# Kernel optimization log

Measured on AMD Instinct MI355X. Metric: run time of the kernel, lower is better.

## Reference

```python
import jax, jax.numpy as jnp
import numpy as np

THETA = 10000.0
NUM_HEADS = 16
MAX_SEQ_LEN = 2048

def _rope_tables(d_k, max_seq_len, theta=THETA):
    dims = jnp.arange(0, d_k, 2, dtype=jnp.float32)
    freqs = 1.0 / theta ** (dims / d_k)
    t = jnp.arange(max_seq_len, dtype=jnp.float32)
    angles = jnp.outer(t, freqs)  # (max_seq_len, d_k//2)
    return jnp.cos(angles), jnp.sin(angles)

def _apply_rope(x, token_positions, cos_tab, sin_tab):
    # x: (..., seq_len, d_k)
    cos = jnp.repeat(cos_tab[token_positions], 2, axis=-1)  # (seq_len, d_k)
    sin = jnp.repeat(sin_tab[token_positions], 2, axis=-1)
    # interleaved rotate-half: (-x1, x0, -x3, x2, ...)
    xp = x.reshape(*x.shape[:-1], -1, 2)
    x_neg = jnp.stack([-xp[..., 1], xp[..., 0]], axis=-1).reshape(x.shape)
    return x * cos + x_neg * sin

def setup_inputs() -> dict:
    key = jax.random.key(0)
    ks = jax.random.split(key, 5)
    B, S, D = 4, 2048, 1024
    scale = 1.0 / np.sqrt(D)
    return {
        "x": jax.random.normal(ks[0], (B, S, D), dtype=jnp.float32),
        "q_proj": jax.random.normal(ks[1], (D, D), dtype=jnp.float32) * scale,
        "k_proj": jax.random.normal(ks[2], (D, D), dtype=jnp.float32) * scale,
        "v_proj": jax.random.normal(ks[3], (D, D), dtype=jnp.float32) * scale,
        "o_proj": jax.random.normal(ks[4], (D, D), dtype=jnp.float32) * scale,
        "token_positions": jnp.arange(S, dtype=jnp.int64),
    }

def reference(x, q_proj, k_proj, v_proj, o_proj, token_positions):
    B, S, D = x.shape
    H = NUM_HEADS
    d_k = D // H
    cos_tab, sin_tab = _rope_tables(d_k, MAX_SEQ_LEN)

    q = (x @ q_proj).reshape(B, S, H, d_k).transpose(0, 2, 1, 3)  # (B,H,S,d_k)
    k = (x @ k_proj).reshape(B, S, H, d_k).transpose(0, 2, 1, 3)
    v = (x @ v_proj).reshape(B, S, H, d_k).transpose(0, 2, 1, 3)

    q = _apply_rope(q, token_positions, cos_tab, sin_tab)
    k = _apply_rope(k, token_positions, cos_tab, sin_tab)

    scores = jnp.einsum('bhqd,bhkd->bhqk', q, k) / jnp.sqrt(jnp.float32(d_k))
    causal = jnp.tril(jnp.ones((S, S), dtype=bool))
    scores = jnp.where(causal, scores, -jnp.inf)
    attn = jax.nn.softmax(scores, axis=-1)
    out = jnp.einsum('bhqk,bhkd->bhqd', attn, v)  # (B,H,S,d_k)
    out = out.transpose(0, 2, 1, 3).reshape(B, S, D)
    return out @ o_proj
```

## Files before the change

### kernel.cpp

```cpp
#include <hip/hip_runtime.h>
#include <hip/hip_bf16.h>
#include <stdint.h>


typedef __attribute__((ext_vector_type(8))) short short8;
typedef __attribute__((ext_vector_type(4))) float floatx4;
typedef __attribute__((ext_vector_type(16))) float floatx16;

#define MFMA16(a,b,c) __builtin_amdgcn_mfma_f32_16x16x32_bf16((a),(b),(c),0,0,0)
#define MFMA32(a,b,c) __builtin_amdgcn_mfma_f32_32x32x16_bf16((a),(b),(c),0,0,0)
#define BAR() __builtin_amdgcn_s_barrier()
#define LGKM0 asm volatile("s_waitcnt lgkmcnt(0)" ::: "memory")
#define VMCNT6 asm volatile("s_waitcnt vmcnt(6)" ::: "memory")

__device__ __forceinline__ uint32_t fbits(float f){ uint32_t u; __builtin_memcpy(&u,&f,4); return u; }
__device__ __forceinline__ unsigned short f2bf(float f) {
    uint32_t u = fbits(f);
    return (unsigned short)((u + 0x7fffu + ((u>>16)&1u)) >> 16);
}
__device__ __forceinline__ float bf2f(unsigned short s){ uint32_t u = (uint32_t)s<<16; float f; __builtin_memcpy(&f,&u,4); return f; }
__device__ __forceinline__ uint32_t pkbf(float lo, float hi) {
#if __has_builtin(__builtin_amdgcn_cvt_pk_bf16_f32)
    auto r = __builtin_amdgcn_cvt_pk_bf16_f32(lo, hi);
    uint32_t u; __builtin_memcpy(&u, &r, sizeof(u));
    return u;
#else
    return __builtin_amdgcn_perm(fbits(hi)+0x8000u, fbits(lo)+0x8000u, 0x07060302u);
#endif
}
__device__ __forceinline__ float fexp2(float x) {
#if __has_builtin(__builtin_amdgcn_exp2f)
    return __builtin_amdgcn_exp2f(x);
#else
    return exp2f(x);
#endif
}

__device__ __forceinline__ void load_lds16(const unsigned short* g, unsigned short* l) {
    __builtin_amdgcn_global_load_lds(
        (const __attribute__((address_space(1))) void*)g,
        (__attribute__((address_space(3))) void*)l, 16, 0, 0);
}

__device__ __forceinline__ bool sniff_f32(const unsigned short* xr) {
    int lane = threadIdx.x & 63;
    int bad = 0;
#pragma unroll
    for (int i = 0; i < 16; i++) {
        float v = bf2f(xr[lane * 16 + i]);
        if (!(__builtin_fabsf(v) < 1e10f)) bad = 1;
    }
    return __ballot(bad != 0) != 0ull;
}

__global__ __launch_bounds__(256) void prep_k(
    const void* __restrict__ x,
    const void* __restrict__ wq, const void* __restrict__ wk,
    const void* __restrict__ wv, const void* __restrict__ wo,
    unsigned short* __restrict__ WT, unsigned short* __restrict__ WoT,
    float2* __restrict__ tab, unsigned short* __restrict__ xb) {
    int blk = blockIdx.x, t = threadIdx.x;
    bool f32 = sniff_f32((const unsigned short*)x);
    if (blk < 4096) {
        __shared__ unsigned short tile[32][33];
        int mat = blk >> 10, r = blk & 1023;
        const void* src = (mat == 0) ? wq : (mat == 1) ? wk : (mat == 2) ? wv : wo;
        unsigned short* dst = (mat < 3) ? (WT + (size_t)mat * 1048576) : WoT;
        int bx = (r & 31) * 32, by = (r >> 5) * 32;
        int tx = t & 31, ty = t >> 5;
#pragma unroll
        for (int j = 0; j < 32; j += 8) {
            size_t idx = (size_t)(by + ty + j) * 1024 + bx + tx;
            float v = f32 ? ((const float*)src)[idx] : bf2f(((const unsigned short*)src)[idx]);
            tile[ty + j][tx] = f2bf(v);
        }
        __syncthreads();
#pragma unroll
        for (int j = 0; j < 32; j += 8)
            dst[(size_t)(bx + ty + j) * 1024 + by + tx] = tile[tx][ty + j];
    } else if (blk < 4352) {
        int i = (blk - 4096) * 256 + t;
        int pos = i >> 5, j = i & 31;
        float freq = exp2f(-(float)(2 * j) * (1.0f / 64.0f) * 13.287712379549449f);
        float a = (float)pos * freq;
        tab[i] = make_float2(cosf(a), sinf(a));
    } else {
        size_t base = (size_t)(blk - 4352) * 2048 + (size_t)t * 8;
        if (f32) {
            const float4* s4 = (const float4*)((const float*)x + base);
            float4 a = s4[0], b = s4[1];
            uint4 o;
            o.x = pkbf(a.x, a.y); o.y = pkbf(a.z, a.w);
            o.z = pkbf(b.x, b.y); o.w = pkbf(b.z, b.w);
            *(uint4*)(xb + base) = o;
        } else {
            *(uint4*)(xb + base) = *(const uint4*)((const unsigned short*)x + base);
        }
    }
}

template <int MODE>
__global__ __launch_bounds__(256, 2) void gemmt(
    const unsigned short* __restrict__ A,
    const unsigned short* __restrict__ Bt,
    void* __restrict__ C0,
    unsigned short* __restrict__ C1,
    unsigned short* __restrict__ C2,
    const float2* __restrict__ tab,
    const unsigned short* __restrict__ xsniff) {
    const int K = 1024;
    extern __shared__ __align__(16) char smraw[];
    unsigned short* SL = (unsigned short*)smraw;

    int t = threadIdx.x;
    int lane = t & 63, w = t >> 6;
    int quad = lane >> 4, l15 = lane & 15;
    int wn = w * 64;

    int nbx = gridDim.x;
    int flat = blockIdx.y * nbx + blockIdx.x;
    int cpx = (nbx * gridDim.y) >> 3;
    int swzid = (flat & 7) * cpx + (flat >> 3);
    int bx = swzid % nbx, by = swzid / nbx;
    int m0 = by * 128, n0 = bx * 256;

    floatx4 acc[8][4];
#pragma unroll
    for (int i = 0; i < 8; i++)
#pragma unroll
        for (int j = 0; j < 4; j++) acc[i][j] = (floatx4){0.f, 0.f, 0.f, 0.f};

    int sg = ((t & 3) ^ ((t >> 3) & 3)) * 8;
    const unsigned short* gA = A + (size_t)(m0 + (t >> 2)) * K + sg;
    const unsigned short* gB = Bt + (size_t)(n0 + (t >> 2)) * K + sg;

    int colsw = (quad ^ ((l15 >> 1) & 3)) * 8;

#pragma unroll
    for (int kt = 0; kt < 2; kt++) {
        unsigned short* Sb = SL + kt * 12288 + w * 512;
        load_lds16(gA + kt * 32, Sb);
        load_lds16(gA + (size_t)64 * K + kt * 32, Sb + 2048);
        load_lds16(gB + kt * 32, Sb + 4096);
        load_lds16(gB + (size_t)64 * K + kt * 32, Sb + 6144);
        load_lds16(gB + (size_t)128 * K + kt * 32, Sb + 8192);
        load_lds16(gB + (size_t)192 * K + kt * 32, Sb + 10240);
    }
    VMCNT6;
    __syncthreads();

    int cur = 0, nxt = 2;
#pragma unroll 1
    for (int kt = 0; kt < 32; kt++) {
        const unsigned short* cA = SL + cur * 12288;
        const unsigned short* cB = SL + cur * 12288 + 4096;
        unsigned short* Sb = SL + nxt * 12288 + w * 512;
        int kc = (kt < 30) ? (kt + 2) : 31;
        size_t ko = (size_t)kc * 32;
        short8 af[4], bf[4];

#pragma unroll
        for (int m = 0; m < 4; m++)
            af[m] = *(const short8*)(cA + (m * 16 + l15) * 32 + colsw);
#pragma unroll
        for (int n = 0; n < 4; n++)
            bf[n] = *(const short8*)(cB + (wn + n * 16 + l15) * 32 + colsw);
        load_lds16(gA + ko, Sb);
        load_lds16(gA + (size_t)64 * K + ko, Sb + 2048);
        load_lds16(gB + ko, Sb + 4096);
        BAR(); LGKM0;
        __builtin_amdgcn_s_setprio(1);
#pragma unroll
        for (int m = 0; m < 4; m++)
#pragma unroll
            for (int n = 0; n < 4; n++) acc[m][n] = MFMA16(af[m], bf[n], acc[m][n]);
        __builtin_amdgcn_s_setprio(0);
        BAR();

#pragma unroll
        for (int m = 0; m < 4; m++)
            af[m] = *(const short8*)(cA + ((m + 4) * 16 + l15) * 32 + colsw);
        load_lds16(gB + (size_t)64 * K + ko, Sb + 6144);
        load_lds16(gB + (size_t)128 * K + ko, Sb + 8192);
        load_lds16(gB + (size_t)192 * K + ko, Sb + 10240);
        BAR(); LGKM0;
        __builtin_amdgcn_s_setprio(1);
#pragma unroll
        for (int m = 0; m < 4; m++)
#pragma unroll
            for (int n = 0; n < 4; n++) acc[m + 4][n] = MFMA16(af[m], bf[n], acc[m + 4][n]);
        __builtin_amdgcn_s_setprio(0);
        VMCNT6;
        BAR();

        cur = (cur == 2) ? 0 : cur + 1;
        nxt = (nxt == 2) ? 0 : nxt + 1;
    }

    bool out_f32 = (MODE == 0) ? sniff_f32(xsniff) : false;
#pragma unroll
    for (int i = 0; i < 8; i++) {
#pragma unroll
        for (int j = 0; j < 4; j++) {
            int col = n0 + wn + j * 16 + l15;
            int row0 = m0 + i * 16 + quad * 4;
            if (MODE == 0) {
#pragma unroll
                for (int r = 0; r < 4; r++) {
                    size_t idx = (size_t)(row0 + r) * 1024 + col;
                    if (out_f32) ((float*)C0)[idx] = acc[i][j][r];
                    else ((unsigned short*)C0)[idx] = f2bf(acc[i][j][r]);
                }
            } else {
                int which = col >> 10, nn = col & 1023;
                int b = row0 >> 11, s0 = row0 & 2047;
                if (which == 2) {
                    int hh = nn >> 6, d = nn & 63;
                    uint32_t lo = pkbf(acc[i][j][0], acc[i][j][1]);
                    uint32_t hi = pkbf(acc[i][j][2], acc[i][j][3]);
                    *(uint64_t*)(C2 + ((size_t)((b * 16 + hh) * 64 + d)) * 2048 + s0) =
                        (uint64_t)lo | ((uint64_t)hi << 32);
                } else {
                    int d = nn & 63;
                    unsigned short* dst = (which == 0) ? (unsigned short*)C0 : C1;
                    float sc = (which == 0) ? 0.18033688011112042f : 1.0f;
#pragma unroll
                    for (int r = 0; r < 4; r++) {
                        int s = s0 + r;
                        float v = acc[i][j][r];
                        float pv = __shfl_xor(v, 1);
                        float2 cs = tab[(s << 5) + (d >> 1)];
                        float o = (d & 1) ? (v * cs.x + pv * cs.y) : (v * cs.x - pv * cs.y);
                        dst[((size_t)(b * 2048 + s)) * 1024 + nn] = f2bf(o * sc);
                    }
                }
            }
        }
    }
}

__global__ __launch_bounds__(512, 4) void flash_k(
    const unsigned short* __restrict__ Qb,
    const unsigned short* __restrict__ Kb,
    const unsigned short* __restrict__ Vt,
    unsigned short* __restrict__ A2) {
    __shared__ __align__(16) char sm[33792];
    unsigned short* Kl = (unsigned short*)sm;
    unsigned short* Vl = (unsigned short*)(sm + 16384);
    float4* Osw = (float4*)sm;
    float*  lsw = (float*)(sm + 32768);

    int bh = blockIdx.x;
    int y = blockIdx.y;
    int qt = (y < 8) ? (15 - y) : (y - 8);
    int b = bh >> 4, h = bh & 15;
    int t = threadIdx.x, lane = t & 63, w = t >> 6;
    int wq = w & 3, wg = w >> 2;
    int l31 = lane & 31, half = lane >> 5;
    size_t base = ((size_t)b * 2048) * 1024 + h * 64;
    int q0w = qt * 128 + wq * 32;

    short8 Qf[4];
#pragma unroll
    for (int ks = 0; ks < 4; ks++)
        Qf[ks] = *(const short8*)(Qb + base + (size_t)(q0w + l31) * 1024 + ks * 16 + half * 8);

    floatx16 O[2];
    O[0] = (floatx16)0.0f; O[1] = (floatx16)0.0f;
    float lsum = 0.f;

    int nk = 2 * (qt + 1);

    int srow = t >> 3, gs = t & 7;
    const unsigned short* kg = Kb + base + (size_t)srow * 1024 + gs * 8;
    const unsigned short* vg = Vt + ((size_t)(bh * 64 + srow)) * 2048 + gs * 8;
    int sw = srow * 64 + ((gs ^ (srow & 7)) * 8);

    short8 rk = *(const short8*)(kg);
    short8 rv = *(const short8*)(vg);

    for (int kt = 0; kt < nk; kt++) {
        int k0 = kt * 64, bf = kt & 1;
        *(short8*)&Kl[bf * 4096 + sw] = rk;
        *(short8*)&Vl[bf * 4096 + sw] = rv;
        __syncthreads();
        if (kt + 1 < nk) {
            size_t ko = (size_t)(kt + 1) * 64;
            rk = *(const short8*)(kg + ko * 1024);
            rv = *(const short8*)(vg + ko);
        }
        int k0mb = k0 + wg * 32;
        if (k0mb < q0w + 32) {
            const unsigned short* Klb = Kl + bf * 4096;
            const unsigned short* Vlb = Vl + bf * 4096;
            short8 Ka[4];
#pragma unroll
            for (int ks = 0; ks < 4; ks++)
                Ka[ks] = *(const short8*)&Klb[(wg * 32 + l31) * 64 +
                                              (((ks * 2 + half) ^ (l31 & 7)) * 8)];
            floatx16 Sc = (floatx16)0.0f;
#pragma unroll
            for (int ks = 0; ks < 4; ks++)
                Sc = MFMA32(Ka[ks], Qf[ks], Sc);

            bool domask = (k0mb + 31 > q0w);
            int thr = q0w + l31 - k0mb - half * 4;
            float p[16];
#pragma unroll
            for (int e = 0; e < 16; e++) {
                float v = fexp2(Sc[e]);
                if (domask) {
                    const int ce = (e & 3) + ((e >> 2) << 3);
                    v = (ce > thr) ? 0.f : v;
                }
                p[e] = v;
            }
            float t0 = (p[0] + p[1]) + (p[2] + p[3]);
            float t1 = (p[4] + p[5]) + (p[6] + p[7]);
            float t2 = (p[8] + p[9]) + (p[10] + p[11]);
            float t3 = (p[12] + p[13]) + (p[14] + p[15]);
            lsum += (t0 + t1) + (t2 + t3);
            uint32_t pkm[8];
#pragma unroll
            for (int jj = 0; jj < 8; jj++)
                pkm[jj] = pkbf(p[2 * jj], p[2 * jj + 1]);

            short8 Va[2][2];
#pragma unroll
            for (int db = 0; db < 2; db++)
#pragma unroll
                for (int ks2 = 0; ks2 < 2; ks2++)
                    Va[db][ks2] = *(const short8*)&Vlb[(db * 32 + l31) * 64 +
                                                       ((((wg * 2 + ks2) * 2 + half) ^ (l31 & 7)) * 8)];
#pragma unroll
            for (int ks2 = 0; ks2 < 2; ks2++) {
                uint32_t p0 = pkm[4 * ks2 + 0];
                uint32_t p1 = pkm[4 * ks2 + 1];
                uint32_t p2 = pkm[4 * ks2 + 2];
                uint32_t p3 = pkm[4 * ks2 + 3];
                uint32_t u = half ? p0 : p2;
                uint32_t v2 = half ? p1 : p3;
                uint32_t ya = (uint32_t)__shfl_xor((int)u, 32);
                uint32_t yb = (uint32_t)__shfl_xor((int)v2, 32);
                union { short8 s; uint32_t q[4]; } bb;
                bb.q[0] = half ? ya : p0;
                bb.q[1] = half ? yb : p1;
                bb.q[2] = half ? p2 : ya;
                bb.q[3] = half ? p3 : yb;
#pragma unroll
                for (int db = 0; db < 2; db++)
                    O[db] = MFMA32(Va[db][ks2], bb.s, O[db]);
            }
        }
    }

    __syncthreads();
    if (w < 4) {
#pragma unroll
        for (int db = 0; db < 2; db++)
#pragma unroll
            for (int g = 0; g < 4; g++)
                Osw[(w * 8 + db * 4 + g) * 64 + lane] =
                    make_float4(O[db][g * 4 + 0], O[db][g * 4 + 1],
                                O[db][g * 4 + 2], O[db][g * 4 + 3]);
        lsw[w * 64 + lane] = lsum;
    }
    __syncthreads();
    if (w >= 4) {
        int wp = w - 4;
#pragma unroll
        for (int db = 0; db < 2; db++)
#pragma unroll
            for (int g = 0; g < 4; g++) {
                float4 o = Osw[(wp * 8 + db * 4 + g) * 64 + lane];
                O[db][g * 4 + 0] += o.x;
                O[db][g * 4 + 1] += o.y;
                O[db][g * 4 + 2] += o.z;
                O[db][g * 4 + 3] += o.w;
            }
        lsum += lsw[wp * 64 + lane];
        float tot = lsum + __shfl_xor(lsum, 32);
        float inv = 1.0f / tot;
        int scol = q0w + l31;
        unsigned short* op = A2 + base + (size_t)scol * 1024;
#pragma unroll
        for (int db = 0; db < 2; db++) {
#pragma unroll
            for (int g = 0; g < 4; g++) {
                int d0 = db * 32 + half * 4 + g * 8;
                float v0 = O[db][g * 4 + 0] * inv;
                float v1 = O[db][g * 4 + 1] * inv;
                float v2 = O[db][g * 4 + 2] * inv;
                float v3 = O[db][g * 4 + 3] * inv;
                uint32_t lo = pkbf(v0, v1), hi = pkbf(v2, v3);
                *(uint64_t*)(op + d0) = (uint64_t)lo | ((uint64_t)hi << 32);
            }
        }
    }
}

extern "C" void kernel_launch(void* const* d_in, const int* in_sizes, int n_in,
                              void* d_out, int out_size, void* d_ws, size_t ws_size,
                              hipStream_t stream) {
    const void* x  = d_in[0];
    const void* wq = d_in[1];
    const void* wk = d_in[2];
    const void* wv = d_in[3];
    const void* wo = d_in[4];

    char* ws = (char*)d_ws;
    unsigned short* WT  = (unsigned short*)(ws);
    unsigned short* WoT = (unsigned short*)(ws + 6291456);
    float2*         tab = (float2*)(ws + 8388608);
    unsigned short* xb  = (unsigned short*)(ws + 8913920);
    unsigned short* Qb  = (unsigned short*)(ws + 8913920 + 16777216ull);
    unsigned short* Kb  = (unsigned short*)(ws + 8913920 + 2ull * 16777216);
    unsigned short* Vt  = (unsigned short*)(ws + 8913920 + 3ull * 16777216);
    unsigned short* A2  = xb;

    (void)hipFuncSetAttribute(reinterpret_cast<const void*>(gemmt<1>),
                              hipFuncAttributeMaxDynamicSharedMemorySize, 73728);
    (void)hipFuncSetAttribute(reinterpret_cast<const void*>(gemmt<0>),
                              hipFuncAttributeMaxDynamicSharedMemorySize, 73728);

    prep_k<<<8448, 256, 0, stream>>>(x, wq, wk, wv, wo, WT, WoT, tab, xb);

    gemmt<1><<<dim3(12, 64), 256, 73728, stream>>>(xb, WT, Qb, Kb, Vt, tab,
                                                   (const unsigned short*)x);
    flash_k<<<dim3(64, 16), 512, 0, stream>>>(Qb, Kb, Vt, A2);
    gemmt<0><<<dim3(4, 64), 256, 73728, stream>>>(A2, WoT, d_out, nullptr, nullptr, tab,
                                                  (const unsigned short*)x);
}
```

Before: 254.0 us.

## Give each flash wave its own query rows instead of splitting keys

The flash attention block now covers 256 query rows, with each of the 8 waves owning 32 rows and walking both 32-key halves of every K/V tile. Before, two wave groups split the key dimension and merged partial outputs through shared memory. Dropping that split removes the final LDS reduction and its barriers, and each K/V tile loaded into LDS is reused across twice as many queries. In exchange there are half as many blocks (512), each wave does more serial work per tile, and causal load imbalance between waves grows.

```diff
diff --git a/kernel.cpp b/kernel.cpp
--- a/kernel.cpp
+++ b/kernel.cpp
@@ -244,21 +244,17 @@
     const unsigned short* __restrict__ Kb,
     const unsigned short* __restrict__ Vt,
     unsigned short* __restrict__ A2) {
-    __shared__ __align__(16) char sm[33792];
-    unsigned short* Kl = (unsigned short*)sm;
-    unsigned short* Vl = (unsigned short*)(sm + 16384);
-    float4* Osw = (float4*)sm;
-    float*  lsw = (float*)(sm + 32768);
+    __shared__ __align__(16) unsigned short Kl[2][64 * 64];
+    __shared__ __align__(16) unsigned short Vl[2][64 * 64];
 
     int bh = blockIdx.x;
     int y = blockIdx.y;
-    int qt = (y < 8) ? (15 - y) : (y - 8);
+    int qt = (y < 4) ? (7 - y) : (y - 4);
     int b = bh >> 4, h = bh & 15;
     int t = threadIdx.x, lane = t & 63, w = t >> 6;
-    int wq = w & 3, wg = w >> 2;
     int l31 = lane & 31, half = lane >> 5;
     size_t base = ((size_t)b * 2048) * 1024 + h * 64;
-    int q0w = qt * 128 + wq * 32;
+    int q0w = qt * 256 + w * 32;
 
     short8 Qf[4];
 #pragma unroll
@@ -269,7 +265,7 @@
     O[0] = (floatx16)0.0f; O[1] = (floatx16)0.0f;
     float lsum = 0.f;
 
-    int nk = 2 * (qt + 1);
+    int nk = 4 * (qt + 1);
 
     int srow = t >> 3, gs = t & 7;
     const unsigned short* kg = Kb + base + (size_t)srow * 1024 + gs * 8;
@@ -281,23 +277,23 @@
 
     for (int kt = 0; kt < nk; kt++) {
         int k0 = kt * 64, bf = kt & 1;
-        *(short8*)&Kl[bf * 4096 + sw] = rk;
-        *(short8*)&Vl[bf * 4096 + sw] = rv;
+        *(short8*)&Kl[bf][sw] = rk;
+        *(short8*)&Vl[bf][sw] = rv;
         __syncthreads();
         if (kt + 1 < nk) {
             size_t ko = (size_t)(kt + 1) * 64;
             rk = *(const short8*)(kg + ko * 1024);
             rv = *(const short8*)(vg + ko);
         }
-        int k0mb = k0 + wg * 32;
-        if (k0mb < q0w + 32) {
-            const unsigned short* Klb = Kl + bf * 4096;
-            const unsigned short* Vlb = Vl + bf * 4096;
+#pragma unroll
+        for (int mb = 0; mb < 2; mb++) {
+            int k0mb = k0 + mb * 32;
+            if (k0mb >= q0w + 32) continue;
             short8 Ka[4];
 #pragma unroll
             for (int ks = 0; ks < 4; ks++)
-                Ka[ks] = *(const short8*)&Klb[(wg * 32 + l31) * 64 +
-                                              (((ks * 2 + half) ^ (l31 & 7)) * 8)];
+                Ka[ks] = *(const short8*)&Kl[bf][(mb * 32 + l31) * 64 +
+                                                 (((ks * 2 + half) ^ (l31 & 7)) * 8)];
             floatx16 Sc = (floatx16)0.0f;
 #pragma unroll
             for (int ks = 0; ks < 4; ks++)
@@ -330,8 +326,8 @@
             for (int db = 0; db < 2; db++)
 #pragma unroll
                 for (int ks2 = 0; ks2 < 2; ks2++)
-                    Va[db][ks2] = *(const short8*)&Vlb[(db * 32 + l31) * 64 +
-                                                       ((((wg * 2 + ks2) * 2 + half) ^ (l31 & 7)) * 8)];
+                    Va[db][ks2] = *(const short8*)&Vl[bf][(db * 32 + l31) * 64 +
+                                                         ((((mb * 2 + ks2) * 2 + half) ^ (l31 & 7)) * 8)];
 #pragma unroll
             for (int ks2 = 0; ks2 < 2; ks2++) {
                 uint32_t p0 = pkm[4 * ks2 + 0];
@@ -354,47 +350,21 @@
         }
     }
 
-    __syncthreads();
-    if (w < 4) {
-#pragma unroll
-        for (int db = 0; db < 2; db++)
-#pragma unroll
-            for (int g = 0; g < 4; g++)
-                Osw[(w * 8 + db * 4 + g) * 64 + lane] =
-                    make_float4(O[db][g * 4 + 0], O[db][g * 4 + 1],
-                                O[db][g * 4 + 2], O[db][g * 4 + 3]);
-        lsw[w * 64 + lane] = lsum;
-    }
-    __syncthreads();
-    if (w >= 4) {
-        int wp = w - 4;
-#pragma unroll
-        for (int db = 0; db < 2; db++)
-#pragma unroll
-            for (int g = 0; g < 4; g++) {
-                float4 o = Osw[(wp * 8 + db * 4 + g) * 64 + lane];
-                O[db][g * 4 + 0] += o.x;
-                O[db][g * 4 + 1] += o.y;
-                O[db][g * 4 + 2] += o.z;
-                O[db][g * 4 + 3] += o.w;
-            }
-        lsum += lsw[wp * 64 + lane];
-        float tot = lsum + __shfl_xor(lsum, 32);
-        float inv = 1.0f / tot;
-        int scol = q0w + l31;
-        unsigned short* op = A2 + base + (size_t)scol * 1024;
-#pragma unroll
-        for (int db = 0; db < 2; db++) {
-#pragma unroll
-            for (int g = 0; g < 4; g++) {
-                int d0 = db * 32 + half * 4 + g * 8;
-                float v0 = O[db][g * 4 + 0] * inv;
-                float v1 = O[db][g * 4 + 1] * inv;
-                float v2 = O[db][g * 4 + 2] * inv;
-                float v3 = O[db][g * 4 + 3] * inv;
-                uint32_t lo = pkbf(v0, v1), hi = pkbf(v2, v3);
-                *(uint64_t*)(op + d0) = (uint64_t)lo | ((uint64_t)hi << 32);
-            }
+    float tot = lsum + __shfl_xor(lsum, 32);
+    float inv = 1.0f / tot;
+    int scol = q0w + l31;
+    unsigned short* op = A2 + base + (size_t)scol * 1024;
+#pragma unroll
+    for (int db = 0; db < 2; db++) {
+#pragma unroll
+        for (int g = 0; g < 4; g++) {
+            int d0 = db * 32 + half * 4 + g * 8;
+            float v0 = O[db][g * 4 + 0] * inv;
+            float v1 = O[db][g * 4 + 1] * inv;
+            float v2 = O[db][g * 4 + 2] * inv;
+            float v3 = O[db][g * 4 + 3] * inv;
+            uint32_t lo = pkbf(v0, v1), hi = pkbf(v2, v3);
+            *(uint64_t*)(op + d0) = (uint64_t)lo | ((uint64_t)hi << 32);
         }
     }
 }
@@ -427,7 +397,7 @@
 
     gemmt<1><<<dim3(12, 64), 256, 73728, stream>>>(xb, WT, Qb, Kb, Vt, tab,
                                                    (const unsigned short*)x);
-    flash_k<<<dim3(64, 16), 512, 0, stream>>>(Qb, Kb, Vt, A2);
+    flash_k<<<dim3(64, 8), 512, 0, stream>>>(Qb, Kb, Vt, A2);
     gemmt<0><<<dim3(4, 64), 256, 73728, stream>>>(A2, WoT, d_out, nullptr, nullptr, tab,
                                                   (const unsigned short*)x);
 }
```

After: 247.0 us, median of 5. 1.03x faster.
